# Kernel optimization log

Measured on AMD Instinct MI355X. Metric: run time of the kernel, lower is better.

The kernel has to match this reference:

```python
import jax, jax.numpy as jnp
import numpy as np

B, N, C = 8, 1024, 768
H = 12
HD = C // H
STAGES = 3
MLP_H = 4 * C
EPS = 1e-5


def _layernorm(x, w, b):
    mu = jnp.mean(x, axis=-1, keepdims=True)
    var = jnp.mean(jnp.square(x - mu), axis=-1, keepdims=True)
    return (x - mu) * jax.lax.rsqrt(var + EPS) * w + b


def setup_inputs() -> dict:
    key = jax.random.key(0)
    ks = jax.random.split(key, 16)
    s = 0.02
    return {
        "x": jax.random.normal(ks[0], (B, N, C), dtype=jnp.float32),
        # stacked per-stage attention params (torch Linear layout: [out, in])
        "qkv_w": jax.random.normal(ks[1], (STAGES, 3 * C, C), dtype=jnp.float32) * s,
        "proj_w": jax.random.normal(ks[2], (STAGES, C, C), dtype=jnp.float32) * s,
        "proj_b": jnp.zeros((STAGES, C), dtype=jnp.float32),
        "ln1_w": jnp.ones((C,), dtype=jnp.float32),
        "ln1_b": jnp.zeros((C,), dtype=jnp.float32),
        "ln2_w": jnp.ones((C,), dtype=jnp.float32),
        "ln2_b": jnp.zeros((C,), dtype=jnp.float32),
        "mlp_w1": jax.random.normal(ks[3], (MLP_H, C), dtype=jnp.float32) * s,
        "mlp_b1": jnp.zeros((MLP_H,), dtype=jnp.float32),
        "mlp_w2": jax.random.normal(ks[4], (C, MLP_H), dtype=jnp.float32) * s,
        "mlp_b2": jnp.zeros((C,), dtype=jnp.float32),
        "focus_w": jnp.ones((STAGES,), dtype=jnp.float32),
    }


def reference(x, qkv_w, proj_w, proj_b, ln1_w, ln1_b, ln2_w, ln2_b,
              mlp_w1, mlp_b1, mlp_w2, mlp_b2, focus_w):
    scale = HD ** -0.5
    h = _layernorm(x, ln1_w, ln1_b)  # shared norm1(x) input to all stages
    attn_out = jnp.zeros_like(x)
    for i in range(STAGES):
        qkv = jnp.einsum('bnc,oc->bno', h, qkv_w[i])  # [B,N,3C], no bias (qkv_bias=False)
        qkv = qkv.reshape(B, N, 3, H, HD).transpose(2, 0, 3, 1, 4)  # [3,B,H,N,HD]
        q, k, v = qkv[0], qkv[1], qkv[2]
        attn = jax.nn.softmax(jnp.einsum('bhnd,bhmd->bhnm', q, k) * scale, axis=-1)
        o = jnp.einsum('bhnm,bhmd->bhnd', attn, v)  # [B,H,N,HD]
        o = o.transpose(0, 2, 1, 3).reshape(B, N, C)
        o = jnp.einsum('bnc,oc->bno', o, proj_w[i]) + proj_b[i]
        attn_out = attn_out + focus_w[i] * o
    x = x + attn_out
    h2 = _layernorm(x, ln2_w, ln2_b)
    h2 = jax.nn.gelu(jnp.einsum('bnc,hc->bnh', h2, mlp_w1) + mlp_b1, approximate=False)
    mlp_out = jnp.einsum('bnh,ch->bnc', h2, mlp_w2) + mlp_b2
    return x + mlp_out
```

## Files before the change

### kernel.cpp

```cpp
#include <hip/hip_runtime.h>
#include <hip/hip_bf16.h>
#include <math.h>

#define B_    8
#define N_    1024
#define C_    768
#define H_    12
#define HD_   64
#define MLPH_ 3072
#define M_ROWS 8192
#define QKV3  6912
#define PK    2304

typedef float  f32x4   __attribute__((ext_vector_type(4)));
typedef float  f32x16  __attribute__((ext_vector_type(16)));
typedef __bf16 bf16x8  __attribute__((ext_vector_type(8)));

__device__ __forceinline__ f32x4 mfma16(bf16x8 a, bf16x8 b, f32x4 c) {
    return __builtin_amdgcn_mfma_f32_16x16x32_bf16(a, b, c, 0, 0, 0);
}
__device__ __forceinline__ f32x16 mfma32(bf16x8 a, bf16x8 b, f32x16 c) {
    return __builtin_amdgcn_mfma_f32_32x32x16_bf16(a, b, c, 0, 0, 0);
}

__device__ __forceinline__ void gl16(const __bf16* g, __bf16* l) {
    __builtin_amdgcn_global_load_lds(
        (const __attribute__((address_space(1))) unsigned int*)g,
        (__attribute__((address_space(3))) unsigned int*)l,
        16, 0, 0);
}

__device__ __forceinline__ unsigned packbf(float a, float b) {
    __bf16 x = (__bf16)a, y = (__bf16)b;
    union { __bf16 h; unsigned short u; } ux, uy;
    ux.h = x; uy.h = y;
    return (unsigned)ux.u | ((unsigned)uy.u << 16);
}

__global__ __launch_bounds__(256) void cast_f32_bf16(const float* __restrict__ in,
                                                     __bf16* __restrict__ out, int n) {
    int i = blockIdx.x * 256 + threadIdx.x;
    if (i < n) out[i] = (__bf16)in[i];
}

__global__ __launch_bounds__(256) void prep_proj_w(const float* __restrict__ pw,
                                                   const float* __restrict__ focus,
                                                   __bf16* __restrict__ out) {
    int i = blockIdx.x * 256 + threadIdx.x;
    int c = i % C_;
    int s = (i / C_) % 3;
    int o = i / PK;
    out[i] = (__bf16)(focus[s] * pw[((size_t)s * C_ + o) * C_ + c]);
}

__global__ __launch_bounds__(256) void ln_to_bf16(const float* __restrict__ x,
                                                  const float* __restrict__ g,
                                                  const float* __restrict__ bta,
                                                  __bf16* __restrict__ out) {
    int row = blockIdx.x;
    const float* xr = x + (size_t)row * C_;
    int t = threadIdx.x;
    float v0 = xr[t], v1 = xr[t + 256], v2 = xr[t + 512];
    float s  = v0 + v1 + v2;
    float s2 = v0 * v0 + v1 * v1 + v2 * v2;
#pragma unroll
    for (int m = 1; m < 64; m <<= 1) { s += __shfl_xor(s, m); s2 += __shfl_xor(s2, m); }
    __shared__ float red[8];
    int w = t >> 6, lane = t & 63;
    if (lane == 0) { red[w] = s; red[4 + w] = s2; }
    __syncthreads();
    s  = red[0] + red[1] + red[2] + red[3];
    s2 = red[4] + red[5] + red[6] + red[7];
    float mu   = s * (1.f / C_);
    float var  = s2 * (1.f / C_) - mu * mu;
    float rstd = rsqrtf(var + 1e-5f);
    __bf16* orow = out + (size_t)row * C_;
    orow[t]       = (__bf16)((v0 - mu) * rstd * g[t]       + bta[t]);
    orow[t + 256] = (__bf16)((v1 - mu) * rstd * g[t + 256] + bta[t + 256]);
    orow[t + 512] = (__bf16)((v2 - mu) * rstd * g[t + 512] + bta[t + 512]);
}

template <int MODE>
__global__ __launch_bounds__(512, 2) void gemm8(
    const __bf16* __restrict__ A, const __bf16* __restrict__ W,
    int M, int N, int K, int ntn,
    __bf16* __restrict__ obf, const float* __restrict__ bias)
{
    __shared__ __bf16 L[2][2][2][16][512];

    const int t = threadIdx.x, lane = t & 63, w = t >> 6;
    const int wm = w >> 2, wn = w & 3;
    const int lo = lane & 15, hi = lane >> 4;

    const int nwg = gridDim.x;
    const int bid = blockIdx.x;
    const int wgid = (bid & 7) * (nwg >> 3) + (bid >> 3);
    const int m0 = (wgid / ntn) * 256, n0 = (wgid % ntn) * 256;

    const int r16 = lane >> 2;
    const int cc  = ((lane & 3) * 8) ^ ((lane >> 1) & 16);

    auto stage = [&](int buf, int kh, int k0) {
        __bf16* la = &L[buf][0][kh][2 * w][0];
        const size_t ra = (size_t)(m0 + 2 * w * 16 + r16) * K + k0 + cc;
        gl16(&A[ra], la);
        gl16(&A[ra + (size_t)16 * K], la + 512);
        __bf16* lb = &L[buf][1][kh][2 * w][0];
        const size_t rb = (size_t)(n0 + 2 * w * 16 + r16) * K + k0 + cc;
        gl16(&W[rb], lb);
        gl16(&W[rb + (size_t)16 * K], lb + 512);
    };

    const int rdoff = lo * 32 + ((hi * 8) ^ ((lo << 1) & 16));

    const int nkt = K >> 6;
    stage(0, 0, 0);
    stage(0, 1, 32);

    f32x4 acc[8][4] = {};

    for (int kt = 0; kt < nkt; ++kt) {
        const int buf = kt & 1;
#pragma unroll
        for (int kh = 0; kh < 2; ++kh) {
            if (kt == nkt - 1 && kh == 1) asm volatile("s_waitcnt vmcnt(0)" ::: "memory");
            else                          asm volatile("s_waitcnt vmcnt(4)" ::: "memory");
            __builtin_amdgcn_s_barrier();
            __builtin_amdgcn_sched_barrier(0);
            if (kt + 1 < nkt) stage(buf ^ 1, kh, (kt + 1) * 64 + kh * 32);

            bf16x8 af[8], bfr[4];
#pragma unroll
            for (int mf = 0; mf < 8; mf++)
                af[mf] = *(const bf16x8*)&L[buf][0][kh][wm * 8 + mf][rdoff];
#pragma unroll
            for (int nf = 0; nf < 4; nf++)
                bfr[nf] = *(const bf16x8*)&L[buf][1][kh][wn * 4 + nf][rdoff];
            asm volatile("s_waitcnt lgkmcnt(0)" ::: "memory");
            __builtin_amdgcn_sched_barrier(0);
            __builtin_amdgcn_s_setprio(1);
#pragma unroll
            for (int mf = 0; mf < 8; mf++)
#pragma unroll
                for (int nf = 0; nf < 4; nf++)
                    acc[mf][nf] = mfma16(af[mf], bfr[nf], acc[mf][nf]);
            __builtin_amdgcn_s_setprio(0);
        }
    }

#pragma unroll
    for (int mf = 0; mf < 8; mf++) {
#pragma unroll
        for (int nf = 0; nf < 4; nf++) {
            const int col = n0 + wn * 64 + nf * 16 + lo;
#pragma unroll
            for (int r = 0; r < 4; r++) {
                const int row = m0 + wm * 128 + mf * 16 + hi * 4 + r;
                const size_t o = (size_t)row * N + col;
                float v = acc[mf][nf][r];
                if (MODE == 0) {
                    obf[o] = (__bf16)v;
                } else {
                    float u = v + bias[col];
                    float ge = 0.5f * u * (1.0f + erff(u * 0.70710678118654752f));
                    obf[o] = (__bf16)ge;
                }
            }
        }
    }
}

template <int MODE>
__global__ __launch_bounds__(256) void gemm_bt(
    const __bf16* __restrict__ A, const __bf16* __restrict__ W,
    int M, int N, int K,
    __bf16* __restrict__ obf, float* __restrict__ of32,
    const float* __restrict__ resid, const float* __restrict__ bias,
    const float* __restrict__ focus_p)
{
    __shared__ __bf16 As[3][128][32];
    __shared__ __bf16 Bs[3][128][32];

    const int t    = threadIdx.x;
    const int lane = t & 63;
    const int w    = t >> 6;
    const int wr   = w >> 1, wc = w & 1;
    const int m0   = blockIdx.y * 128, n0 = blockIdx.x * 128;
    const int lo   = lane & 15;

    const int srow = lane >> 2;
    const int scol = (((lane & 3) ^ ((lane >> 3) & 3))) * 8;
    const int rcol = ((((lane >> 4) & 3) ^ ((lane >> 1) & 3))) * 8;

    auto stage = [&](int buf, int k0) {
#pragma unroll
        for (int i = 0; i < 2; i++) {
            const int chunk = w * 2 + i;
            const int row   = chunk * 16 + srow;
            gl16(&A[(size_t)(m0 + row) * K + k0 + scol], &As[buf][chunk * 16][0]);
            gl16(&W[(size_t)(n0 + row) * K + k0 + scol], &Bs[buf][chunk * 16][0]);
        }
    };

    const int nT = K >> 5;
    stage(0, 0);
    stage(1, 32);
    stage(2, 64);

    f32x4 acc[4][4] = {};
    int cur = 0;
    for (int tt = 0; tt < nT; ++tt) {
        const int rem = nT - tt;
        if (rem > 2)       asm volatile("s_waitcnt vmcnt(8)" ::: "memory");
        else if (rem == 2) asm volatile("s_waitcnt vmcnt(4)" ::: "memory");
        else               asm volatile("s_waitcnt vmcnt(0)" ::: "memory");
        __builtin_amdgcn_s_barrier();
        __builtin_amdgcn_sched_barrier(0);

        bf16x8 af[4], bfr[4];
#pragma unroll
        for (int mi = 0; mi < 4; mi++) af[mi]  = *(const bf16x8*)&As[cur][wr * 64 + mi * 16 + lo][rcol];
#pragma unroll
        for (int ni = 0; ni < 4; ni++) bfr[ni] = *(const bf16x8*)&Bs[cur][wc * 64 + ni * 16 + lo][rcol];
#pragma unroll
        for (int mi = 0; mi < 4; mi++)
#pragma unroll
            for (int ni = 0; ni < 4; ni++)
                acc[mi][ni] = mfma16(af[mi], bfr[ni], acc[mi][ni]);

        asm volatile("s_waitcnt lgkmcnt(0)" ::: "memory");
        __builtin_amdgcn_s_barrier();
        if (tt + 3 < nT) stage(cur, (tt + 3) * 32);
        cur = (cur == 2) ? 0 : cur + 1;
    }

    float f0 = 0.f, f1 = 0.f, f2 = 0.f;
    if (MODE == 1) { f0 = focus_p[0]; f1 = focus_p[1]; f2 = focus_p[2]; }

#pragma unroll
    for (int mi = 0; mi < 4; mi++) {
#pragma unroll
        for (int ni = 0; ni < 4; ni++) {
            int col = n0 + wc * 64 + ni * 16 + lo;
#pragma unroll
            for (int r = 0; r < 4; r++) {
                int row = m0 + wr * 64 + mi * 16 + (lane >> 4) * 4 + r;
                size_t o = (size_t)row * N + col;
                float v = acc[mi][ni][r];
                if (MODE == 1) {
                    float be = f0 * bias[col] + f1 * bias[col + C_] + f2 * bias[col + 2 * C_];
                    of32[o] = resid[o] + v + be;
                } else {
                    of32[o] = resid[o] + v + bias[col];
                }
            }
        }
    }
}

__global__ __launch_bounds__(256) void attn_kernel(const __bf16* __restrict__ qkv,
                                                   __bf16* __restrict__ obuf) {
    const int bid  = blockIdx.x;
    const int idx  = bid >> 3;
    const int grp  = (bid & 7) * 36 + (idx >> 3);
    const int qt   = idx & 7;
    const int s    = grp / 96;
    const int rem  = grp % 96;
    const int b    = rem / 12;
    const int h    = rem % 12;
    const int q0   = qt * 128;

    const int t = threadIdx.x, lane = t & 63, w = t >> 6;
    const int l31 = lane & 31, hi1 = lane >> 5;

    __shared__ __bf16 Kf[4096];
    __shared__ __bf16 Vf[4096];
    __shared__ float  Lsm[128];

    const size_t rs = QKV3;
    const __bf16* qb = qkv + (size_t)b * N_ * rs + (size_t)s * PK + h * HD_;
    const __bf16* kb = qb + C_;
    const __bf16* vb = qb + 2 * C_;

    const float cexp = 0.18033688011112042f;

    bf16x8 aq[4];
#pragma unroll
    for (int dk = 0; dk < 4; dk++) {
        aq[dk] = *(const bf16x8*)(qb + (size_t)(q0 + w * 32 + l31) * rs + dk * 16 + hi1 * 8);
#pragma unroll
        for (int j = 0; j < 8; j++) aq[dk][j] = (__bf16)((float)aq[dk][j] * cexp);
    }

    f32x16 oacc[2] = {};
    float lsum = 0.f;

    int4 kreg[2]; uint4 vreg[2];
    auto load_tile = [&](int k0) {
#pragma unroll
        for (int p = 0; p < 2; p++) {
            int id = p * 256 + t;
            int kr = id >> 3, d0 = (id & 7) * 8;
            kreg[p] = *(const int4*)(kb + (size_t)(k0 + kr) * rs + d0);
            int kr2 = id & 63, d2 = ((id >> 6) * 8);
            vreg[p] = *(const uint4*)(vb + (size_t)(k0 + kr2) * rs + d2);
        }
    };
    load_tile(0);

    for (int kt = 0; kt < 16; kt++) {
        __syncthreads();
#pragma unroll
        for (int p = 0; p < 2; p++) {
            int id = p * 256 + t;
            int chunk = (id & 7) * 64 + (id >> 3);
            int c = chunk ^ (id & 7);
            *(int4*)&Kf[c * 8] = kreg[p];
        }
        {
            int k8 = lane >> 3, par = lane & 1, koff = lane & 6;
#pragma unroll
            for (int p = 0; p < 2; p++) {
                int d2 = ((p * 256 + t) >> 6) * 8;
#pragma unroll
                for (int i = 0; i < 4; i++) {
                    unsigned mw = vreg[p][i];
                    unsigned pw = (unsigned)__builtin_amdgcn_mov_dpp((int)mw, 0xB1, 0xF, 0xF, true);
                    unsigned out = par ? ((pw >> 16) | (mw & 0xFFFF0000u))
                                       : ((mw & 0xFFFFu) | (pw << 16));
                    int d = d2 + 2 * i + par;
                    int chunk = k8 * 64 + d;
                    int c = chunk ^ k8;
                    *(unsigned*)&Vf[c * 8 + koff] = out;
                }
            }
        }
        __syncthreads();
        if (kt < 15) load_tile((kt + 1) * 64);

        f32x16 sacc[2] = {};
#pragma unroll
        for (int ks = 0; ks < 2; ks++)
#pragma unroll
            for (int dk = 0; dk < 4; dk++) {
                int d8 = dk * 2 + hi1;
                int c = (d8 * 64 + ks * 32 + l31) ^ d8;
                bf16x8 kf = *(const bf16x8*)&Kf[c * 8];
                sacc[ks] = mfma32(kf, aq[dk], sacc[ks]);
            }

#pragma unroll
        for (int ks = 0; ks < 2; ks++) {
            float pe[16];
#pragma unroll
            for (int r = 0; r < 16; r++) {
                pe[r] = __builtin_amdgcn_exp2f(sacc[ks][r]);
                lsum += pe[r];
            }
            unsigned pk[8];
#pragma unroll
            for (int i = 0; i < 8; i++) pk[i] = packbf(pe[2 * i], pe[2 * i + 1]);

            unsigned a0 = pk[0], a2 = pk[2], a1 = pk[1], a3 = pk[3];
            {
                auto r0 = __builtin_amdgcn_permlane32_swap((int)a0, (int)a2, false, false);
                a0 = (unsigned)r0[0]; a2 = (unsigned)r0[1];
                auto r1 = __builtin_amdgcn_permlane32_swap((int)a1, (int)a3, false, false);
                a1 = (unsigned)r1[0]; a3 = (unsigned)r1[1];
            }
            unsigned b0 = pk[4], b2 = pk[6], b1 = pk[5], b3 = pk[7];
            {
                auto r0 = __builtin_amdgcn_permlane32_swap((int)b0, (int)b2, false, false);
                b0 = (unsigned)r0[0]; b2 = (unsigned)r0[1];
                auto r1 = __builtin_amdgcn_permlane32_swap((int)b1, (int)b3, false, false);
                b1 = (unsigned)r1[0]; b3 = (unsigned)r1[1];
            }
            union { unsigned u[4]; bf16x8 v; } fr0, fr1;
            fr0.u[0] = a0; fr0.u[1] = a1; fr0.u[2] = a2; fr0.u[3] = a3;
            fr1.u[0] = b0; fr1.u[1] = b1; fr1.u[2] = b2; fr1.u[3] = b3;

#pragma unroll
            for (int f = 0; f < 2; f++) {
                bf16x8 pa = f ? fr1.v : fr0.v;
#pragma unroll
                for (int dh = 0; dh < 2; dh++) {
                    int k8 = ks * 4 + f * 2 + hi1;
                    int c = (k8 * 64 + dh * 32 + l31) ^ k8;
                    bf16x8 vf = *(const bf16x8*)&Vf[c * 8];
                    oacc[dh] = mfma32(pa, vf, oacc[dh]);
                }
            }
        }
    }

    float ls2 = lsum + __shfl_xor(lsum, 32);
    if (lane < 32) Lsm[w * 32 + lane] = ls2;
    f32x4 Ls[4];
#pragma unroll
    for (int g = 0; g < 4; g++)
        Ls[g] = *(const f32x4*)&Lsm[w * 32 + 8 * g + 4 * hi1];

    __bf16* obase = obuf + ((size_t)b * N_ + q0 + w * 32) * PK + (size_t)s * C_ + h * HD_ + l31;
#pragma unroll
    for (int g = 0; g < 4; g++)
#pragma unroll
        for (int i = 0; i < 4; i++) {
            float inv = 1.0f / Ls[g][i];
            int q_local = i + 8 * g + 4 * hi1;
            __bf16* orow = obase + (size_t)q_local * PK;
            orow[0]  = (__bf16)(oacc[0][4 * g + i] * inv);
            orow[32] = (__bf16)(oacc[1][4 * g + i] * inv);
        }
}

extern "C" void kernel_launch(void* const* d_in, const int* in_sizes, int n_in,
                              void* d_out, int out_size, void* d_ws, size_t ws_size,
                              hipStream_t stream) {
    const float* x      = (const float*)d_in[0];
    const float* qkv_w  = (const float*)d_in[1];
    const float* proj_w = (const float*)d_in[2];
    const float* proj_b = (const float*)d_in[3];
    const float* ln1_w  = (const float*)d_in[4];
    const float* ln1_b  = (const float*)d_in[5];
    const float* ln2_w  = (const float*)d_in[6];
    const float* ln2_b  = (const float*)d_in[7];
    const float* mlp_w1 = (const float*)d_in[8];
    const float* mlp_b1 = (const float*)d_in[9];
    const float* mlp_w2 = (const float*)d_in[10];
    const float* mlp_b2 = (const float*)d_in[11];
    const float* focus  = (const float*)d_in[12];
    float* out = (float*)d_out;

    char* ws = (char*)d_ws;
    size_t off = 0;
    auto alloc = [&](size_t bytes) {
        char* p = ws + off;
        off += (bytes + 255) & ~(size_t)255;
        return p;
    };
    __bf16* h1   = (__bf16*)alloc((size_t)M_ROWS * C_ * 2);
    __bf16* qkvb = (__bf16*)alloc((size_t)M_ROWS * QKV3 * 2);
    __bf16* ob   = (__bf16*)alloc((size_t)M_ROWS * PK * 2);
    float*  x1   = (float*) alloc((size_t)M_ROWS * C_ * 4);
    __bf16* wq   = (__bf16*)alloc((size_t)QKV3 * C_ * 2);
    __bf16* wp   = (__bf16*)alloc((size_t)C_ * PK * 2);
    __bf16* w1   = (__bf16*)alloc((size_t)MLPH_ * C_ * 2);
    __bf16* w2   = (__bf16*)alloc((size_t)C_ * MLPH_ * 2);
    if (off > ws_size) return;
    __bf16* h2  = h1;
    __bf16* hid = qkvb;

    const int nq = QKV3 * C_;
    const int np = C_ * PK;
    const int n1 = MLPH_ * C_;
    cast_f32_bf16<<<(nq + 255) / 256, 256, 0, stream>>>(qkv_w, wq, nq);
    prep_proj_w<<<(np + 255) / 256, 256, 0, stream>>>(proj_w, focus, wp);
    cast_f32_bf16<<<(n1 + 255) / 256, 256, 0, stream>>>(mlp_w1, w1, n1);
    cast_f32_bf16<<<(n1 + 255) / 256, 256, 0, stream>>>(mlp_w2, w2, n1);

    ln_to_bf16<<<M_ROWS, 256, 0, stream>>>(x, ln1_w, ln1_b, h1);

    gemm8<0><<<(M_ROWS / 256) * (QKV3 / 256), 512, 0, stream>>>(
        h1, wq, M_ROWS, QKV3, C_, QKV3 / 256, qkvb, nullptr);

    attn_kernel<<<3 * B_ * H_ * (N_ / 128), 256, 0, stream>>>(qkvb, ob);

    gemm_bt<1><<<dim3(C_ / 128, M_ROWS / 128), 256, 0, stream>>>(
        ob, wp, M_ROWS, C_, PK, nullptr, x1, x, proj_b, focus);

    ln_to_bf16<<<M_ROWS, 256, 0, stream>>>(x1, ln2_w, ln2_b, h2);

    gemm8<2><<<(M_ROWS / 256) * (MLPH_ / 256), 512, 0, stream>>>(
        h2, w1, M_ROWS, MLPH_, C_, MLPH_ / 256, hid, mlp_b1);

    gemm_bt<3><<<dim3(C_ / 128, M_ROWS / 128), 256, 0, stream>>>(
        hid, w2, M_ROWS, C_, MLPH_, nullptr, out, x1, mlp_b2, nullptr);
}
```

Before: 490.3 us.

## Merge weight-cast kernels into one launch and raise MFMA wave priority in attention

```diff
diff --git a/kernel.cpp b/kernel.cpp
--- a/kernel.cpp
+++ b/kernel.cpp
@@ -37,20 +37,29 @@
     return (unsigned)ux.u | ((unsigned)uy.u << 16);
 }
 
-__global__ __launch_bounds__(256) void cast_f32_bf16(const float* __restrict__ in,
-                                                     __bf16* __restrict__ out, int n) {
+__global__ __launch_bounds__(256) void prep_weights(
+    const float* __restrict__ qkv_w, const float* __restrict__ proj_w,
+    const float* __restrict__ mlp_w1, const float* __restrict__ mlp_w2,
+    const float* __restrict__ focus,
+    __bf16* __restrict__ wq, __bf16* __restrict__ wp,
+    __bf16* __restrict__ w1, __bf16* __restrict__ w2) {
+    const int nq = QKV3 * C_;
+    const int np = C_ * PK;
+    const int n1 = MLPH_ * C_;
     int i = blockIdx.x * 256 + threadIdx.x;
-    if (i < n) out[i] = (__bf16)in[i];
-}
-
-__global__ __launch_bounds__(256) void prep_proj_w(const float* __restrict__ pw,
-                                                   const float* __restrict__ focus,
-                                                   __bf16* __restrict__ out) {
-    int i = blockIdx.x * 256 + threadIdx.x;
-    int c = i % C_;
-    int s = (i / C_) % 3;
-    int o = i / PK;
-    out[i] = (__bf16)(focus[s] * pw[((size_t)s * C_ + o) * C_ + c]);
+    if (i < nq) { wq[i] = (__bf16)qkv_w[i]; return; }
+    i -= nq;
+    if (i < np) {
+        int c = i % C_;
+        int st = (i / C_) % 3;
+        int o = i / PK;
+        wp[i] = (__bf16)(focus[st] * proj_w[((size_t)st * C_ + o) * C_ + c]);
+        return;
+    }
+    i -= np;
+    if (i < n1) { w1[i] = (__bf16)mlp_w1[i]; return; }
+    i -= n1;
+    w2[i] = (__bf16)mlp_w2[i];
 }
 
 __global__ __launch_bounds__(256) void ln_to_bf16(const float* __restrict__ x,
@@ -339,6 +348,7 @@
         if (kt < 15) load_tile((kt + 1) * 64);
 
         f32x16 sacc[2] = {};
+        __builtin_amdgcn_s_setprio(1);
 #pragma unroll
         for (int ks = 0; ks < 2; ks++)
 #pragma unroll
@@ -348,6 +358,7 @@
                 bf16x8 kf = *(const bf16x8*)&Kf[c * 8];
                 sacc[ks] = mfma32(kf, aq[dk], sacc[ks]);
             }
+        __builtin_amdgcn_s_setprio(0);
 
 #pragma unroll
         for (int ks = 0; ks < 2; ks++) {
@@ -382,6 +393,7 @@
 #pragma unroll
             for (int f = 0; f < 2; f++) {
                 bf16x8 pa = f ? fr1.v : fr0.v;
+                __builtin_amdgcn_s_setprio(1);
 #pragma unroll
                 for (int dh = 0; dh < 2; dh++) {
                     int k8 = ks * 4 + f * 2 + hi1;
@@ -389,6 +401,7 @@
                     bf16x8 vf = *(const bf16x8*)&Vf[c * 8];
                     oacc[dh] = mfma32(pa, vf, oacc[dh]);
                 }
+                __builtin_amdgcn_s_setprio(0);
             }
         }
     }
@@ -450,13 +463,9 @@
     __bf16* h2  = h1;
     __bf16* hid = qkvb;
 
-    const int nq = QKV3 * C_;
-    const int np = C_ * PK;
-    const int n1 = MLPH_ * C_;
-    cast_f32_bf16<<<(nq + 255) / 256, 256, 0, stream>>>(qkv_w, wq, nq);
-    prep_proj_w<<<(np + 255) / 256, 256, 0, stream>>>(proj_w, focus, wp);
-    cast_f32_bf16<<<(n1 + 255) / 256, 256, 0, stream>>>(mlp_w1, w1, n1);
-    cast_f32_bf16<<<(n1 + 255) / 256, 256, 0, stream>>>(mlp_w2, w2, n1);
+    const int ntot = QKV3 * C_ + C_ * PK + 2 * MLPH_ * C_;
+    prep_weights<<<ntot / 256, 256, 0, stream>>>(
+        qkv_w, proj_w, mlp_w1, mlp_w2, focus, wq, wp, w1, w2);
 
     ln_to_bf16<<<M_ROWS, 256, 0, stream>>>(x, ln1_w, ln1_b, h1);
 
```

Result: slower. 531.9 us (+8.5%).
